# Optimization experiments

Measured on AMD Instinct MI355X. Metric: run time of the kernel, lower is better.

The kernel has to match this reference:

```python
import jax, jax.numpy as jnp
import numpy as np

EPS = 1e-6

def rmsnorm(x, w):
    return x * jax.lax.rsqrt(jnp.mean(x * x, axis=-1, keepdims=True) + EPS) * w

def apply_rope(q, k, freqs_cis):
    # q: (B,T,H,D), k: (B,T,Hkv,D), freqs_cis: (T, D//2, 2) = (cos, sin)
    cos = freqs_cis[None, :, None, :, 0]
    sin = freqs_cis[None, :, None, :, 1]
    def rot(t):
        tr = t.reshape(*t.shape[:-1], t.shape[-1] // 2, 2)
        re, im = tr[..., 0], tr[..., 1]
        out = jnp.stack([re * cos - im * sin, re * sin + im * cos], axis=-1)
        return out.reshape(t.shape)
    return rot(q), rot(k)

def swiglu(x, w1, w2, w3):
    # torch Linear: y = x @ W.T ; SwiGLU: (silu(x W1^T) * (x W3^T)) W2^T
    return (jax.nn.silu(x @ w1.T) * (x @ w3.T)) @ w2.T

def setup_inputs() -> dict:
    key = jax.random.key(0)
    ks = jax.random.split(key, 16)
    B, T, C = 4, 2048, 1024
    H, Hkv, D = 16, 4, 64
    E, Hh = 8, 512
    s = 0.02
    # rotary frequencies (theta=10000)
    inv_freq = 1.0 / (10000.0 ** (np.arange(0, D, 2, dtype=np.float32) / D))
    t = np.arange(T, dtype=np.float32)
    ang = np.outer(t, inv_freq)  # (T, D/2)
    freqs_cis = jnp.asarray(np.stack([np.cos(ang), np.sin(ang)], axis=-1))
    return {
        "x": jax.random.normal(ks[0], (B, T, C), jnp.float32),
        "freqs_cis": freqs_cis,
        "norm1_w": jnp.ones((C,), jnp.float32),
        "wq": jax.random.normal(ks[1], (C, C), jnp.float32) * s,
        "wk": jax.random.normal(ks[2], (Hkv * D, C), jnp.float32) * s,
        "wv": jax.random.normal(ks[3], (Hkv * D, C), jnp.float32) * s,
        "wo": jax.random.normal(ks[4], (C, C), jnp.float32) * s,
        "norm2_w": jnp.ones((C,), jnp.float32),
        "gate_w": jax.random.normal(ks[5], (E, C), jnp.float32) * s,
        "sw1": jax.random.normal(ks[6], (Hh, C), jnp.float32) * s,
        "sw2": jax.random.normal(ks[7], (C, Hh), jnp.float32) * s,
        "sw3": jax.random.normal(ks[8], (Hh, C), jnp.float32) * s,
        "ew1": jax.random.normal(ks[9], (E, Hh, C), jnp.float32) * s,
        "ew2": jax.random.normal(ks[10], (E, C, Hh), jnp.float32) * s,
        "ew3": jax.random.normal(ks[11], (E, Hh, C), jnp.float32) * s,
    }

def reference(x, freqs_cis, norm1_w, wq, wk, wv, wo, norm2_w, gate_w,
              sw1, sw2, sw3, ew1, ew2, ew3):
    B, T, C = x.shape
    H, Hkv = 16, 4
    D = C // H
    n_rep = H // Hkv
    E, top_k = gate_w.shape[0], 2

    # --- attention (GQA + RoPE, causal) ---
    xn = rmsnorm(x, norm1_w)
    q = (xn @ wq.T).reshape(B, T, H, D)
    k = (xn @ wk.T).reshape(B, T, Hkv, D)
    v = (xn @ wv.T).reshape(B, T, Hkv, D)
    q, k = apply_rope(q, k, freqs_cis)
    k = jnp.repeat(k, n_rep, axis=2)
    v = jnp.repeat(v, n_rep, axis=2)
    q, k, v = (t.transpose(0, 2, 1, 3) for t in (q, k, v))  # (B,H,T,D)
    scores = jnp.einsum("bhqd,bhkd->bhqk", q, k) / jnp.sqrt(jnp.float32(D))
    causal = jnp.tril(jnp.ones((T, T), bool))
    scores = jnp.where(causal, scores, jnp.finfo(scores.dtype).min)
    attn = jax.nn.softmax(scores, axis=-1)
    y = jnp.einsum("bhqk,bhkd->bhqd", attn, v)
    y = y.transpose(0, 2, 1, 3).reshape(B, T, C) @ wo.T
    x = x + y

    # --- MoE FFN ---
    xn2 = rmsnorm(x, norm2_w)
    shared = swiglu(xn2, sw1, sw2, sw3)
    router_logits = xn2 @ gate_w.T  # (B,T,E)
    top_logits, top_idx = jax.lax.top_k(router_logits, top_k)
    top_w = jax.nn.softmax(top_logits, axis=-1)  # (B,T,top_k)
    # dense per-expert weight, zero where not selected (same math as masked loop)
    w_full = jnp.sum(jax.nn.one_hot(top_idx, E, dtype=xn2.dtype) * top_w[..., None], axis=-2)  # (B,T,E)
    h = jax.nn.silu(jnp.einsum("btc,ehc->bteh", xn2, ew1)) * jnp.einsum("btc,ehc->bteh", xn2, ew3)
    expert_out = jnp.einsum("bteh,ech,bte->btc", h, ew2, w_full)
    x = x + shared + expert_out
    return x, router_logits
```

## Files before the change

### kernel.cpp

```cpp
#include <hip/hip_runtime.h>
#include <math.h>

typedef __bf16 bf16;
typedef bf16 bf16x8 __attribute__((ext_vector_type(8)));
typedef bf16 bf16x4 __attribute__((ext_vector_type(4)));
typedef float f32x4 __attribute__((ext_vector_type(4)));

#define B_    4
#define T_    2048
#define C_    1024
#define H_    16
#define HKV_  4
#define D_    64
#define HH_   512
#define E_    8
#define MTOK  (B_*T_)
#define MAXTILES 144
#define ROWCAP  (MAXTILES*128)

__device__ __forceinline__ f32x4 mfma16(bf16x8 a, bf16x8 b, f32x4 c) {
  return __builtin_amdgcn_mfma_f32_16x16x32_bf16(a, b, c, 0, 0, 0);
}

#define GLOAD16(gsrc, ldst) \
  __builtin_amdgcn_global_load_lds((const __attribute__((address_space(1))) void*)(gsrc), \
                                   (__attribute__((address_space(3))) void*)(ldst), 16, 0, 0)

#define XCD_SWZ(bx, by) \
  const int _nw  = gridDim.x * gridDim.y; \
  const int _bid = blockIdx.y * gridDim.x + blockIdx.x; \
  const int _swz = (_bid & 7) * (_nw >> 3) + (_bid >> 3); \
  const int bx = _swz % gridDim.x; \
  const int by = _swz / gridDim.x;

struct CastSegs {
  const float* src[10];
  bf16* dst[10];
  int prefix[11];
};
__global__ void cast_all_kernel(CastSegs cs) {
  int i = blockIdx.x * 256 + threadIdx.x;
  if (i >= cs.prefix[10]) return;
  int seg = 0;
  #pragma unroll
  for (int k = 0; k < 9; ++k) if (i >= cs.prefix[k+1]) seg = k+1;
  int j = i - cs.prefix[seg];
  float4 v = reinterpret_cast<const float4*>(cs.src[seg])[j];
  bf16x4 o = { (bf16)v.x, (bf16)v.y, (bf16)v.z, (bf16)v.w };
  reinterpret_cast<bf16x4*>(cs.dst[seg])[j] = o;
}

__global__ void rmsnorm_cast_kernel(const float* __restrict__ x, const float* __restrict__ w,
                                    bf16* __restrict__ out) {
  int row = blockIdx.x;
  const float4* xr = reinterpret_cast<const float4*>(x + (size_t)row * C_);
  float4 v = xr[threadIdx.x];
  float ss = v.x*v.x + v.y*v.y + v.z*v.z + v.w*v.w;
  #pragma unroll
  for (int off = 32; off > 0; off >>= 1) ss += __shfl_down(ss, off);
  __shared__ float red[4];
  if ((threadIdx.x & 63) == 0) red[threadIdx.x >> 6] = ss;
  __syncthreads();
  float tot = red[0] + red[1] + red[2] + red[3];
  float scale = rsqrtf(tot * (1.0f / C_) + 1e-6f);
  float4 wv = reinterpret_cast<const float4*>(w)[threadIdx.x];
  bf16x4 o = { (bf16)(v.x*scale*wv.x), (bf16)(v.y*scale*wv.y),
               (bf16)(v.z*scale*wv.z), (bf16)(v.w*scale*wv.w) };
  reinterpret_cast<bf16x4*>(out + (size_t)row * C_)[threadIdx.x] = o;
}

template<int EPI>
__global__ __launch_bounds__(256, 4)
void gemm_bt(const bf16* __restrict__ A, const bf16* __restrict__ W,
             float* __restrict__ D, const float* __restrict__ SRC,
             const float* __restrict__ RS, int rs_stride,
             int M, int N, int K)
{
  XCD_SWZ(bx, by);
  __shared__ __align__(16) bf16 As[128*32];
  __shared__ __align__(16) bf16 Bs[128*32];
  const int tid  = threadIdx.x;
  const int lane = tid & 63;
  const int wid  = tid >> 6;
  const int wr = wid >> 1, wc = wid & 1;
  const int m0 = by * 128;
  const int n0 = bx * 128;
  const int r  = lane & 15;
  const int kg = lane >> 4;
  const int srow = wid * 32 + (lane >> 2);
  const int scol = (lane & 3) * 8;
  const bf16* gA = A + (size_t)(m0 + srow) * K + scol;
  const bf16* gB = W + (size_t)(n0 + srow) * K + scol;
  bf16* lA = As + wid * 1024;
  bf16* lB = Bs + wid * 1024;

  f32x4 acc[4][4];
  #pragma unroll
  for (int i = 0; i < 4; ++i)
    #pragma unroll
    for (int j = 0; j < 4; ++j) acc[i][j] = f32x4{0.f,0.f,0.f,0.f};

  for (int kk = 0; kk < K; kk += 32) {
    GLOAD16(gA + kk,          lA);
    GLOAD16(gA + 16*K + kk,   lA + 512);
    GLOAD16(gB + kk,          lB);
    GLOAD16(gB + 16*K + kk,   lB + 512);
    __syncthreads();
    bf16x8 a[4], b[4];
    #pragma unroll
    for (int i = 0; i < 4; ++i)
      a[i] = *reinterpret_cast<const bf16x8*>(&As[(wr*64 + i*16 + r)*32 + kg*8]);
    #pragma unroll
    for (int j = 0; j < 4; ++j)
      b[j] = *reinterpret_cast<const bf16x8*>(&Bs[(wc*64 + j*16 + r)*32 + kg*8]);
    #pragma unroll
    for (int i = 0; i < 4; ++i)
      #pragma unroll
      for (int j = 0; j < 4; ++j)
        acc[i][j] = mfma16(a[i], b[j], acc[i][j]);
    __syncthreads();
  }
  const int dr = kg * 4;
  #pragma unroll
  for (int i = 0; i < 4; ++i)
    #pragma unroll
    for (int j = 0; j < 4; ++j)
      #pragma unroll
      for (int rr = 0; rr < 4; ++rr) {
        int m = m0 + wr*64 + i*16 + dr + rr;
        int n = n0 + wc*64 + j*16 + r;
        size_t idx = (size_t)m * N + n;
        float v = acc[i][j][rr];
        if (EPI == 0)      D[idx] = v;
        else if (EPI == 1) D[idx] = SRC[idx] + v;
        else if (EPI == 2) D[idx] += v;
        else               D[idx] += RS[(size_t)m * rs_stride] * v;
      }
}

__global__ __launch_bounds__(256, 4)
void gemm_qkv(const bf16* __restrict__ A, const bf16* __restrict__ W,
              const float* __restrict__ fr,
              bf16* __restrict__ qb, bf16* __restrict__ kb, bf16* __restrict__ vb)
{
  const int K = C_;
  XCD_SWZ(bx, by);
  __shared__ __align__(16) bf16 As[128*32];
  __shared__ __align__(16) bf16 Bs[128*32];
  const int tid  = threadIdx.x;
  const int lane = tid & 63;
  const int wid  = tid >> 6;
  const int wr = wid >> 1, wc = wid & 1;
  const int m0 = by * 128;
  const int n0 = bx * 128;
  const int r  = lane & 15;
  const int kg = lane >> 4;
  const int srow = wid * 32 + (lane >> 2);
  const int scol = (lane & 3) * 8;
  const bf16* gA = A + (size_t)(m0 + srow) * K + scol;
  const bf16* gB = W + (size_t)(n0 + srow) * K + scol;
  bf16* lA = As + wid * 1024;
  bf16* lB = Bs + wid * 1024;

  f32x4 acc[4][4];
  #pragma unroll
  for (int i = 0; i < 4; ++i)
    #pragma unroll
    for (int j = 0; j < 4; ++j) acc[i][j] = f32x4{0.f,0.f,0.f,0.f};

  for (int kk = 0; kk < K; kk += 32) {
    GLOAD16(gA + kk,          lA);
    GLOAD16(gA + 16*K + kk,   lA + 512);
    GLOAD16(gB + kk,          lB);
    GLOAD16(gB + 16*K + kk,   lB + 512);
    __syncthreads();
    bf16x8 a[4], b[4];
    #pragma unroll
    for (int i = 0; i < 4; ++i)
      a[i] = *reinterpret_cast<const bf16x8*>(&As[(wr*64 + i*16 + r)*32 + kg*8]);
    #pragma unroll
    for (int j = 0; j < 4; ++j)
      b[j] = *reinterpret_cast<const bf16x8*>(&Bs[(wc*64 + j*16 + r)*32 + kg*8]);
    #pragma unroll
    for (int i = 0; i < 4; ++i)
      #pragma unroll
      for (int j = 0; j < 4; ++j)
        acc[i][j] = mfma16(a[i], b[j], acc[i][j]);
    __syncthreads();
  }
  const float QSCALE = 0.125f * 1.44269504088896340736f;
  const int dr = kg * 4;
  #pragma unroll
  for (int i = 0; i < 4; ++i)
    #pragma unroll
    for (int j = 0; j < 4; ++j)
      #pragma unroll
      for (int rr = 0; rr < 4; ++rr) {
        int mrow = m0 + wr*64 + i*16 + dr + rr;
        int b  = mrow >> 11, t = mrow & (T_ - 1);
        int n  = n0 + wc*64 + j*16 + r;
        float v = acc[i][j][rr];
        float p = __shfl_xor(v, 1);
        if (n < 1024) {
          float c = fr[t*64 + (n & 62)], s = fr[t*64 + (n & 62) + 1];
          float ov = (n & 1) ? (p*s + v*c) : (v*c - p*s);
          qb[((size_t)(b*H_ + (n >> 6)) * T_ + t) * 64 + (n & 63)] = (bf16)(ov * QSCALE);
        } else if (n < 1280) {
          float c = fr[t*64 + (n & 62)], s = fr[t*64 + (n & 62) + 1];
          float ov = (n & 1) ? (p*s + v*c) : (v*c - p*s);
          kb[((size_t)(b*HKV_ + ((n - 1024) >> 6)) * T_ + t) * 64 + (n & 63)] = (bf16)ov;
        } else {
          vb[((size_t)(b*HKV_ + ((n - 1280) >> 6)) * T_ + t) * 64 + (n & 63)] = (bf16)v;
        }
      }
}

__global__ __launch_bounds__(256, 4)
void gemm_up_all(const bf16* __restrict__ A,
                 const bf16* __restrict__ SW1, const bf16* __restrict__ SW3,
                 const bf16* __restrict__ EW1, const bf16* __restrict__ EW3,
                 size_t wstride, bf16* __restrict__ sb, bf16* __restrict__ sbm,
                 const int* __restrict__ tb, const int* __restrict__ tki)
{
  const int K = C_;
  XCD_SWZ(bx, by);
  const int y = by;
  const bool dense = (y < 64);
  const bf16 *W1, *W3;
  int rowbase;
  bf16* outp;
  if (dense) {
    W1 = SW1; W3 = SW3; rowbase = y * 128; outp = sb;
  } else {
    int ye = y - 64;
    if (ye >= tb[16]) return;
    int g = 0;
    while (ye >= tb[g + 1]) ++g;
    W1 = EW1 + (size_t)(g & 7) * wstride;
    W3 = EW3 + (size_t)(g & 7) * wstride;
    rowbase = ye * 128; outp = sbm;
  }

  __shared__ __align__(16) bf16 As[128*32];
  __shared__ __align__(16) bf16 W1s[64*32];
  __shared__ __align__(16) bf16 W3s[64*32];
  const int tid  = threadIdx.x;
  const int lane = tid & 63;
  const int wid  = tid >> 6;
  const int wr = wid >> 1, wc = wid & 1;
  const int n0 = bx * 64;
  const int r  = lane & 15;
  const int kg = lane >> 4;

  const int sArow = wid * 32 + (lane >> 2);
  int arow0 = dense ? (rowbase + sArow)      : tki[rowbase + sArow];
  int arow1 = dense ? (rowbase + sArow + 16) : tki[rowbase + sArow + 16];
  const int sWrow = n0 + wid * 16 + (lane >> 2);
  const int scol  = (lane & 3) * 8;
  const bf16* gA0 = A  + (size_t)arow0 * K + scol;
  const bf16* gA1 = A  + (size_t)arow1 * K + scol;
  const bf16* gW1 = W1 + (size_t)sWrow * K + scol;
  const bf16* gW3 = W3 + (size_t)sWrow * K + scol;
  bf16* lA  = As  + wid * 1024;
  bf16* lW1 = W1s + wid * 512;
  bf16* lW3 = W3s + wid * 512;

  f32x4 acc1[4][2], acc3[4][2];
  #pragma unroll
  for (int i = 0; i < 4; ++i)
    #pragma unroll
    for (int j = 0; j < 2; ++j) { acc1[i][j] = f32x4{0.f,0.f,0.f,0.f}; acc3[i][j] = f32x4{0.f,0.f,0.f,0.f}; }

  for (int kk = 0; kk < K; kk += 32) {
    GLOAD16(gA0 + kk,       lA);
    GLOAD16(gA1 + kk,       lA + 512);
    GLOAD16(gW1 + kk,       lW1);
    GLOAD16(gW3 + kk,       lW3);
    __syncthreads();
    bf16x8 a[4], w1f[2], w3f[2];
    #pragma unroll
    for (int i = 0; i < 4; ++i)
      a[i] = *reinterpret_cast<const bf16x8*>(&As[(wr*64 + i*16 + r)*32 + kg*8]);
    #pragma unroll
    for (int j = 0; j < 2; ++j) {
      w1f[j] = *reinterpret_cast<const bf16x8*>(&W1s[(wc*32 + j*16 + r)*32 + kg*8]);
      w3f[j] = *reinterpret_cast<const bf16x8*>(&W3s[(wc*32 + j*16 + r)*32 + kg*8]);
    }
    #pragma unroll
    for (int i = 0; i < 4; ++i)
      #pragma unroll
      for (int j = 0; j < 2; ++j) {
        acc1[i][j] = mfma16(a[i], w1f[j], acc1[i][j]);
        acc3[i][j] = mfma16(a[i], w3f[j], acc3[i][j]);
      }
    __syncthreads();
  }
  const int dr = kg * 4;
  #pragma unroll
  for (int i = 0; i < 4; ++i)
    #pragma unroll
    for (int j = 0; j < 2; ++j)
      #pragma unroll
      for (int rr = 0; rr < 4; ++rr) {
        int row = rowbase + wr*64 + i*16 + dr + rr;
        int n = n0 + wc*32 + j*16 + r;
        float v1 = acc1[i][j][rr];
        float v3 = acc3[i][j][rr];
        outp[(size_t)row * HH_ + n] = (bf16)(v1 / (1.f + __expf(-v1)) * v3);
      }
}

__global__ __launch_bounds__(256, 4)
void gemm_down_all(const bf16* __restrict__ Asb, const bf16* __restrict__ Asbm,
                   const bf16* __restrict__ SW2, const bf16* __restrict__ EW2,
                   size_t wstride, float* __restrict__ out, bf16* __restrict__ dwn,
                   const int* __restrict__ tb)
{
  const int K = HH_;
  XCD_SWZ(bx, by);
  const int y = by;
  const bool dense = (y < 64);
  const bf16 *A, *W;
  int rowbase;
  if (dense) {
    A = Asb; W = SW2; rowbase = y * 128;
  } else {
    int ye = y - 64;
    if (ye >= tb[16]) return;
    int g = 0;
    while (ye >= tb[g + 1]) ++g;
    A = Asbm; W = EW2 + (size_t)(g & 7) * wstride;
    rowbase = ye * 128;
  }

  __shared__ __align__(16) bf16 As[128*32];
  __shared__ __align__(16) bf16 Bs[128*32];
  const int tid  = threadIdx.x;
  const int lane = tid & 63;
  const int wid  = tid >> 6;
  const int wr = wid >> 1, wc = wid & 1;
  const int n0 = bx * 128;
  const int r  = lane & 15;
  const int kg = lane >> 4;

  const int srow = wid * 32 + (lane >> 2);
  const int scol = (lane & 3) * 8;
  const bf16* gA = A + (size_t)(rowbase + srow) * K + scol;
  const bf16* gB = W + (size_t)(n0 + srow) * K + scol;
  bf16* lA = As + wid * 1024;
  bf16* lB = Bs + wid * 1024;

  f32x4 acc[4][4];
  #pragma unroll
  for (int i = 0; i < 4; ++i)
    #pragma unroll
    for (int j = 0; j < 4; ++j) acc[i][j] = f32x4{0.f,0.f,0.f,0.f};

  for (int kk = 0; kk < K; kk += 32) {
    GLOAD16(gA + kk,          lA);
    GLOAD16(gA + 16*K + kk,   lA + 512);
    GLOAD16(gB + kk,          lB);
    GLOAD16(gB + 16*K + kk,   lB + 512);
    __syncthreads();
    bf16x8 a[4], b[4];
    #pragma unroll
    for (int i = 0; i < 4; ++i)
      a[i] = *reinterpret_cast<const bf16x8*>(&As[(wr*64 + i*16 + r)*32 + kg*8]);
    #pragma unroll
    for (int j = 0; j < 4; ++j)
      b[j] = *reinterpret_cast<const bf16x8*>(&Bs[(wc*64 + j*16 + r)*32 + kg*8]);
    #pragma unroll
    for (int i = 0; i < 4; ++i)
      #pragma unroll
      for (int j = 0; j < 4; ++j)
        acc[i][j] = mfma16(a[i], b[j], acc[i][j]);
    __syncthreads();
  }
  const int dr = kg * 4;
  #pragma unroll
  for (int i = 0; i < 4; ++i)
    #pragma unroll
    for (int j = 0; j < 4; ++j)
      #pragma unroll
      for (int rr = 0; rr < 4; ++rr) {
        int row = rowbase + wr*64 + i*16 + dr + rr;
        int n = n0 + wc*64 + j*16 + r;
        float v = acc[i][j][rr];
        if (dense) out[(size_t)row * C_ + n] += v;
        else       dwn[(size_t)row * C_ + n] = (bf16)v;
      }
}

__global__ void moe_scatter_kernel(const bf16* __restrict__ dwn,
                                   const int* __restrict__ t2s,
                                   const float* __restrict__ t2w,
                                   float* __restrict__ out)
{
  int t = blockIdx.x;
  int c = threadIdx.x;
  int s0 = t2s[2*t], s1 = t2s[2*t+1];
  float w0 = t2w[2*t], w1 = t2w[2*t+1];
  bf16x4 a = reinterpret_cast<const bf16x4*>(dwn + (size_t)s0 * C_)[c];
  bf16x4 b = reinterpret_cast<const bf16x4*>(dwn + (size_t)s1 * C_)[c];
  float4* o = reinterpret_cast<float4*>(out + (size_t)t * C_);
  float4 v = o[c];
  v.x += w0 * (float)a[0] + w1 * (float)b[0];
  v.y += w0 * (float)a[1] + w1 * (float)b[1];
  v.z += w0 * (float)a[2] + w1 * (float)b[2];
  v.w += w0 * (float)a[3] + w1 * (float)b[3];
  o[c] = v;
}

__global__ void transpose_vb_kernel(const bf16* __restrict__ vb, bf16* __restrict__ vt) {
  int idx = blockIdx.x * 256 + threadIdx.x;
  const int total = B_ * HKV_ * 64 * T_;
  if (idx >= total) return;
  int t   = idx & (T_ - 1);
  int d   = (idx >> 11) & 63;
  int kvh = (idx >> 17) & 3;
  int b   = idx >> 19;
  vt[idx] = vb[((size_t)(b*HKV_ + kvh) * T_ + t) * 64 + d];
}

__global__ __launch_bounds__(256, 2)
void flash_attn_kernel(const bf16* __restrict__ Q, const bf16* __restrict__ K,
                       const bf16* __restrict__ VT, bf16* __restrict__ Y)
{
  __shared__ __align__(16) bf16 Klds[64*64];
  __shared__ __align__(16) bf16 Vlds[64*64];
  __shared__ bf16 Plds[4][2][16][72];
  const int tid  = threadIdx.x;
  const int lane = tid & 63;
  const int wid  = tid >> 6;
  const int bid  = blockIdx.x;
  const int gw   = (bid & 7) * 64 + (bid >> 3);
  const int i    = gw & 31;
  const int kvh  = (gw >> 5) & 3;
  const int b    = gw >> 7;
  const int h    = kvh * 4 + wid;
  const int r = lane & 15;
  const int g = lane >> 4;

  const bf16* kptr = K  + ((size_t)(b*HKV_ + kvh) * T_) * 64;
  const bf16* vptr = VT + ((size_t)(b*HKV_ + kvh) * 64) * T_;

  const int srow  = tid >> 3;
  const int schnk = (tid & 7) ^ (srow & 7);
  bf16* kd0 = Klds + wid * 512;
  bf16* kd1 = Klds + 2048 + wid * 512;
  bf16* vd0 = Vlds + wid * 512;
  bf16* vd1 = Vlds + 2048 + wid * 512;

  const int swz0 = ((g    ) ^ (r & 7)) * 8;
  const int swz4 = ((g + 4) ^ (r & 7)) * 8;

  bf16x8 ones;
  #pragma unroll
  for (int z = 0; z < 8; ++z) ones[z] = (bf16)1.0f;

  #pragma unroll
  for (int pi = 0; pi < 2; ++pi) {
    const int qt = pi == 0 ? (63 - i) : i;
    const int qbase = qt * 32;
    const bf16* qptr = Q + ((size_t)(b*H_ + h) * T_ + qbase) * 64;

    bf16x8 aq[2][2];
    #pragma unroll
    for (int u = 0; u < 2; ++u) {
      aq[u][0] = *reinterpret_cast<const bf16x8*>(qptr + (size_t)(u*16 + r) * 64 + g*8);
      aq[u][1] = *reinterpret_cast<const bf16x8*>(qptr + (size_t)(u*16 + r) * 64 + 32 + g*8);
    }

    f32x4 o[2][4], ol[2];
    #pragma unroll
    for (int u = 0; u < 2; ++u) {
      ol[u] = f32x4{0.f,0.f,0.f,0.f};
      #pragma unroll
      for (int q = 0; q < 4; ++q) o[u][q] = f32x4{0.f,0.f,0.f,0.f};
    }

    for (int k0 = 0; k0 < qbase + 32; k0 += 64) {
      GLOAD16(kptr + (size_t)(k0 + srow)      * 64 + schnk*8, kd0);
      GLOAD16(kptr + (size_t)(k0 + 32 + srow) * 64 + schnk*8, kd1);
      GLOAD16(vptr + (size_t)srow        * T_ + k0 + schnk*8, vd0);
      GLOAD16(vptr + (size_t)(32 + srow) * T_ + k0 + schnk*8, vd1);
      __syncthreads();
      f32x4 s[2][4];
      __builtin_amdgcn_s_setprio(1);
      #pragma unroll
      for (int c = 0; c < 4; ++c) {
        const bf16* kb = &Klds[(c*16 + r) * 64];
        bf16x8 kf0 = *reinterpret_cast<const bf16x8*>(kb + swz0);
        bf16x8 kf1 = *reinterpret_cast<const bf16x8*>(kb + swz4);
        #pragma unroll
        for (int u = 0; u < 2; ++u) {
          s[u][c] = f32x4{0.f,0.f,0.f,0.f};
          s[u][c] = mfma16(aq[u][0], kf0, s[u][c]);
          s[u][c] = mfma16(aq[u][1], kf1, s[u][c]);
        }
      }
      __builtin_amdgcn_s_setprio(0);
      #pragma unroll
      for (int u = 0; u < 2; ++u) {
        if (k0 + 63 > qbase + u*16) {
          #pragma unroll
          for (int c = 0; c < 4; ++c)
            #pragma unroll
            for (int rr = 0; rr < 4; ++rr) {
              int q = qbase + u*16 + g*4 + rr;
              int j = k0 + c*16 + r;
              if (j > q) s[u][c][rr] = -__builtin_inff();
            }
        }
      }
      #pragma unroll
      for (int u = 0; u < 2; ++u)
        #pragma unroll
        for (int c = 0; c < 4; ++c)
          #pragma unroll
          for (int rr = 0; rr < 4; ++rr)
            Plds[wid][u][g*4+rr][c*16+r] = (bf16)__builtin_amdgcn_exp2f(s[u][c][rr]);
      bf16x8 pa[2][2];
      #pragma unroll
      for (int u = 0; u < 2; ++u) {
        pa[u][0] = *reinterpret_cast<const bf16x8*>(&Plds[wid][u][r][g*8]);
        pa[u][1] = *reinterpret_cast<const bf16x8*>(&Plds[wid][u][r][32 + g*8]);
      }
      __builtin_amdgcn_s_setprio(1);
      #pragma unroll
      for (int dt = 0; dt < 4; ++dt) {
        const bf16* vb = &Vlds[(dt*16 + r) * 64];
        bf16x8 vf0 = *reinterpret_cast<const bf16x8*>(vb + swz0);
        bf16x8 vf1 = *reinterpret_cast<const bf16x8*>(vb + swz4);
        #pragma unroll
        for (int u = 0; u < 2; ++u) {
          o[u][dt] = mfma16(pa[u][0], vf0, o[u][dt]);
          o[u][dt] = mfma16(pa[u][1], vf1, o[u][dt]);
        }
      }
      #pragma unroll
      for (int u = 0; u < 2; ++u) {
        ol[u] = mfma16(pa[u][0], ones, ol[u]);
        ol[u] = mfma16(pa[u][1], ones, ol[u]);
      }
      __builtin_amdgcn_s_setprio(0);
      __syncthreads();
    }
    #pragma unroll
    for (int u = 0; u < 2; ++u)
      #pragma unroll
      for (int rr = 0; rr < 4; ++rr) {
        float inv = 1.0f / ol[u][rr];
        int t = qbase + u*16 + g*4 + rr;
        bf16* yrow = Y + ((size_t)(b*T_ + t)) * C_ + h*64;
        #pragma unroll
        for (int dt = 0; dt < 4; ++dt)
          yrow[dt*16 + r] = (bf16)(o[u][dt][rr] * inv);
      }
  }
}

__global__ void rms2_router_kernel(const float* __restrict__ x2, const float* __restrict__ nw,
                                   const float* __restrict__ gwf,
                                   bf16* __restrict__ xn_out,
                                   float* __restrict__ logits_out,
                                   int* __restrict__ t2i, float* __restrict__ t2w)
{
  int t = blockIdx.x * 4 + (threadIdx.x >> 6);
  int lane = threadIdx.x & 63;
  const float4* xr = reinterpret_cast<const float4*>(x2 + (size_t)t * C_) + lane * 4;
  float4 v[4];
  float ss = 0.f;
  #pragma unroll
  for (int i = 0; i < 4; ++i) {
    v[i] = xr[i];
    ss += v[i].x*v[i].x + v[i].y*v[i].y + v[i].z*v[i].z + v[i].w*v[i].w;
  }
  #pragma unroll
  for (int off = 32; off > 0; off >>= 1) ss += __shfl_xor(ss, off);
  float scale = rsqrtf(ss * (1.0f / C_) + 1e-6f);
  const float4* nr = reinterpret_cast<const float4*>(nw) + lane * 4;
  float xn[16];
  #pragma unroll
  for (int i = 0; i < 4; ++i) {
    float4 wv = nr[i];
    xn[4*i+0] = v[i].x * scale * wv.x;
    xn[4*i+1] = v[i].y * scale * wv.y;
    xn[4*i+2] = v[i].z * scale * wv.z;
    xn[4*i+3] = v[i].w * scale * wv.w;
  }
  {
    bf16x8 o0, o1;
    #pragma unroll
    for (int i = 0; i < 8; ++i) { o0[i] = (bf16)xn[i]; o1[i] = (bf16)xn[8+i]; }
    bf16x8* dst = reinterpret_cast<bf16x8*>(xn_out + (size_t)t * C_ + lane * 16);
    dst[0] = o0;
    dst[1] = o1;
  }
  float lg[8];
  #pragma unroll
  for (int e = 0; e < 8; ++e) {
    const float4* gr = reinterpret_cast<const float4*>(gwf + (size_t)e * C_) + lane * 4;
    float d = 0.f;
    #pragma unroll
    for (int i = 0; i < 4; ++i) {
      float4 gv = gr[i];
      d += xn[4*i+0]*gv.x + xn[4*i+1]*gv.y + xn[4*i+2]*gv.z + xn[4*i+3]*gv.w;
    }
    #pragma unroll
    for (int off = 1; off < 64; off <<= 1) d += __shfl_xor(d, off);
    lg[e] = d;
  }
  if (lane == 0) {
    #pragma unroll
    for (int e = 0; e < 8; ++e) logits_out[(size_t)t*8 + e] = lg[e];
    int i0 = 0; float b0 = lg[0];
    #pragma unroll
    for (int e = 1; e < 8; ++e) if (lg[e] > b0) { b0 = lg[e]; i0 = e; }
    int i1 = -1; float b1 = -__builtin_inff();
    #pragma unroll
    for (int e = 0; e < 8; ++e) if (e != i0 && lg[e] > b1) { b1 = lg[e]; i1 = e; }
    float w0s = 1.f / (1.f + __expf(b1 - b0));
    float w1s = 1.f - w0s;
    t2i[2*t] = i0;  t2i[2*t+1] = i1;
    t2w[2*t] = w0s; t2w[2*t+1] = w1s;
  }
}

__global__ void moe_build_kernel(const int* __restrict__ t2i, const float* __restrict__ t2w,
                                 int* __restrict__ cnt, int* __restrict__ tb,
                                 int* __restrict__ tki, float* __restrict__ tkw,
                                 int* __restrict__ t2s)
{
  __shared__ int lcnt[16], lbase[17], lcur[16];
  const int tid = threadIdx.x;
  if (tid < 16) { lcnt[tid] = 0; lcur[tid] = 0; }
  __syncthreads();
  for (int t = tid; t < MTOK; t += 1024) {
    atomicAdd(&lcnt[t2i[2*t]],     1);
    atomicAdd(&lcnt[8 + t2i[2*t+1]], 1);
  }
  __syncthreads();
  if (tid == 0) {
    int acc = 0;
    for (int g = 0; g < 16; ++g) { lbase[g] = acc; acc += (lcnt[g] + 127) >> 7; }
    lbase[16] = acc;
    for (int g = 0; g <= 16; ++g) tb[g] = lbase[g];
  }
  if (tid < 16) cnt[tid] = lcnt[tid];
  __syncthreads();
  for (int t = tid; t < MTOK; t += 1024) {
    #pragma unroll
    for (int j = 0; j < 2; ++j) {
      int g = 8*j + t2i[2*t + j];
      int p = atomicAdd(&lcur[g], 1);
      int slot = lbase[g] * 128 + p;
      tki[slot] = t;
      tkw[slot] = t2w[2*t + j];
      t2s[2*t + j] = slot;
    }
  }
  __syncthreads();
  {
    int g = tid >> 6, lane = tid & 63;
    int cs = lcnt[g];
    int ce = (cs + 127) & ~127;
    for (int p = cs + lane; p < ce; p += 64) {
      int slot = lbase[g] * 128 + p;
      tki[slot] = 0;
      tkw[slot] = 0.f;
    }
  }
}

__global__ void silu_mul_kernel(const float* __restrict__ a, const float* __restrict__ bsrc,
                                bf16* __restrict__ out, int n4)
{
  int i = blockIdx.x * 256 + threadIdx.x;
  if (i >= n4) return;
  float4 av = reinterpret_cast<const float4*>(a)[i];
  float4 bv = reinterpret_cast<const float4*>(bsrc)[i];
  bf16x4 o = { (bf16)(av.x / (1.f + __expf(-av.x)) * bv.x),
               (bf16)(av.y / (1.f + __expf(-av.y)) * bv.y),
               (bf16)(av.z / (1.f + __expf(-av.z)) * bv.z),
               (bf16)(av.w / (1.f + __expf(-av.w)) * bv.w) };
  reinterpret_cast<bf16x4*>(out)[i] = o;
}

__global__ void build_wfull_kernel(const int* __restrict__ t2i, const float* __restrict__ t2w,
                                   float* __restrict__ wfull) {
  int t = blockIdx.x * 256 + threadIdx.x;
  if (t >= MTOK) return;
  #pragma unroll
  for (int e = 0; e < 8; ++e) wfull[(size_t)t*8 + e] = 0.f;
  wfull[(size_t)t*8 + t2i[2*t]]   = t2w[2*t];
  wfull[(size_t)t*8 + t2i[2*t+1]] = t2w[2*t+1];
}

extern "C" void kernel_launch(void* const* d_in, const int* in_sizes, int n_in,
                              void* d_out, int out_size, void* d_ws, size_t ws_size,
                              hipStream_t stream)
{
  const float* x    = (const float*)d_in[0];
  const float* fr   = (const float*)d_in[1];
  const float* n1w  = (const float*)d_in[2];
  const float* wq   = (const float*)d_in[3];
  const float* wk   = (const float*)d_in[4];
  const float* wv   = (const float*)d_in[5];
  const float* wo   = (const float*)d_in[6];
  const float* n2w  = (const float*)d_in[7];
  const float* gw   = (const float*)d_in[8];
  const float* sw1  = (const float*)d_in[9];
  const float* sw2  = (const float*)d_in[10];
  const float* sw3  = (const float*)d_in[11];
  const float* ew1  = (const float*)d_in[12];
  const float* ew2  = (const float*)d_in[13];
  const float* ew3  = (const float*)d_in[14];

  float* out    = (float*)d_out;
  float* logits = out + (size_t)MTOK * C_;

  char* ws = (char*)d_ws;
  size_t off = 0;
  auto alloc = [&](size_t bytes) { size_t o = off; off += (bytes + 255) & ~(size_t)255; return o; };

  bf16* wq_b  = (bf16*)(ws + alloc((size_t)C_*C_*2));
  bf16* wk_b  = (bf16*)(ws + alloc((size_t)HKV_*D_*C_*2));
  bf16* wv_b  = (bf16*)(ws + alloc((size_t)HKV_*D_*C_*2));
  bf16* wo_b  = (bf16*)(ws + alloc((size_t)C_*C_*2));
  bf16* sw1_b = (bf16*)(ws + alloc((size_t)HH_*C_*2));
  bf16* sw3_b = (bf16*)(ws + alloc((size_t)HH_*C_*2));
  bf16* sw2_b = (bf16*)(ws + alloc((size_t)C_*HH_*2));
  bf16* ew1_b = (bf16*)(ws + alloc((size_t)E_*HH_*C_*2));
  bf16* ew2_b = (bf16*)(ws + alloc((size_t)E_*C_*HH_*2));
  bf16* ew3_b = (bf16*)(ws + alloc((size_t)E_*HH_*C_*2));
  bf16* xn_b  = (bf16*)(ws + alloc((size_t)MTOK*C_*2));
  float* wfull= (float*)(ws + alloc((size_t)MTOK*E_*4));
  int*   t2i  = (int*)  (ws + alloc((size_t)MTOK*2*4));
  float* t2w  = (float*)(ws + alloc((size_t)MTOK*2*4));
  int*   t2s  = (int*)  (ws + alloc((size_t)MTOK*2*4));
  int*   tki  = (int*)  (ws + alloc((size_t)ROWCAP*4));
  float* tkw  = (float*)(ws + alloc((size_t)ROWCAP*4));
  int*   cnt  = (int*)  (ws + alloc(32*4));
  int*   tb   = (int*)  (ws + alloc(32*4));

  const size_t POOLSZ = 75497472;
  size_t poolbase = alloc(POOLSZ);
  char* pool = ws + poolbase;
  bf16* qb = (bf16*)(pool);
  bf16* kb = (bf16*)(pool + 33554432);
  bf16* vb = (bf16*)(pool + 41943040);
  bf16* vT = (bf16*)(pool + 50331648);
  bf16* yb = (bf16*)(pool + 58720256);
  bf16* sb  = (bf16*)(pool);
  bf16* sbm = (bf16*)(pool + 8388608);
  bf16* dwn = (bf16*)(pool + 8388608 + 18874368);
  float* g1 = (float*)pool;
  float* g3 = g1 + (size_t)MTOK*HH_;
  bf16*  sbf = (bf16*)(pool + 58720256);

  bool sparse_ok = (ws_size >= off);

  {
    CastSegs cs;
    const float* srcs[10] = { wq, wk, wv, wo, sw1, sw3, sw2, ew1, ew2, ew3 };
    bf16* dsts[10] = { wq_b, wk_b, wv_b, wo_b, sw1_b, sw3_b, sw2_b, ew1_b, ew2_b, ew3_b };
    int n4s[10] = { C_*C_/4, HKV_*D_*C_/4, HKV_*D_*C_/4, C_*C_/4,
                    HH_*C_/4, HH_*C_/4, C_*HH_/4,
                    E_*HH_*C_/4, E_*C_*HH_/4, E_*HH_*C_/4 };
    int acc = 0;
    for (int k = 0; k < 10; ++k) { cs.src[k] = srcs[k]; cs.dst[k] = dsts[k]; cs.prefix[k] = acc; acc += n4s[k]; }
    cs.prefix[10] = acc;
    cast_all_kernel<<<(acc + 255)/256, 256, 0, stream>>>(cs);
  }

  rmsnorm_cast_kernel<<<MTOK, 256, 0, stream>>>(x, n1w, xn_b);

  gemm_qkv<<<dim3(1536/128, MTOK/128), 256, 0, stream>>>(xn_b, wq_b, fr, qb, kb, vb);
  transpose_vb_kernel<<<(B_*HKV_*64*T_)/256, 256, 0, stream>>>(vb, vT);

  flash_attn_kernel<<<B_*HKV_*(T_/64), 256, 0, stream>>>(qb, kb, vT, yb);

  gemm_bt<1><<<dim3(C_/128, MTOK/128), 256, 0, stream>>>(yb, wo_b, out, x, nullptr, 0, MTOK, C_, C_);

  rms2_router_kernel<<<MTOK/4, 256, 0, stream>>>(out, n2w, gw, xn_b, logits, t2i, t2w);

  if (sparse_ok) {
    moe_build_kernel<<<1, 1024, 0, stream>>>(t2i, t2w, cnt, tb, tki, tkw, t2s);
    gemm_up_all<<<dim3(HH_/64, 64 + MAXTILES), 256, 0, stream>>>(xn_b,
        sw1_b, sw3_b, ew1_b, ew3_b, (size_t)HH_*C_, sb, sbm, tb, tki);
    gemm_down_all<<<dim3(C_/128, 64 + MAXTILES), 256, 0, stream>>>(sb, sbm,
        sw2_b, ew2_b, (size_t)C_*HH_, out, dwn, tb);
    moe_scatter_kernel<<<MTOK, 256, 0, stream>>>(dwn, t2s, t2w, out);
  } else {
    gemm_up_all<<<dim3(HH_/64, 64), 256, 0, stream>>>(xn_b,
        sw1_b, sw3_b, ew1_b, ew3_b, (size_t)HH_*C_, sb, sbm, tb, tki);
    gemm_bt<2><<<dim3(C_/128, MTOK/128), 256, 0, stream>>>(sb, sw2_b, out, nullptr, nullptr, 0, MTOK, C_, HH_);
    build_wfull_kernel<<<MTOK/256, 256, 0, stream>>>(t2i, t2w, wfull);
    for (int e = 0; e < E_; ++e) {
      const bf16* e1 = ew1_b + (size_t)e * HH_ * C_;
      const bf16* e3 = ew3_b + (size_t)e * HH_ * C_;
      const bf16* e2 = ew2_b + (size_t)e * C_ * HH_;
      gemm_bt<0><<<dim3(HH_/128, MTOK/128), 256, 0, stream>>>(xn_b, e1, g1, nullptr, nullptr, 0, MTOK, HH_, C_);
      gemm_bt<0><<<dim3(HH_/128, MTOK/128), 256, 0, stream>>>(xn_b, e3, g3, nullptr, nullptr, 0, MTOK, HH_, C_);
      silu_mul_kernel<<<((MTOK*HH_/4) + 255)/256, 256, 0, stream>>>(g1, g3, sbf, MTOK*HH_/4);
      gemm_bt<3><<<dim3(C_/128, MTOK/128), 256, 0, stream>>>(sbf, e2, out, nullptr, wfull + e, E_, MTOK, C_, HH_);
    }
  }
}
```

Measured before the change: 371.2 us.

## Double K-tile depth to 64 with XOR-swizzled LDS layout in all GEMMs

All four GEMM kernels now stage a K-slice of 64 per iteration instead of 32, which halves the number of barrier pairs and global-to-LDS rounds per output tile. The LDS rows widen to 64 elements and use an XOR swizzle of the 16-byte chunk index by row, applied on both the store and the fragment reads, to avoid bank conflicts. The cost is doubled shared memory per block, which may lower occupancy under the 4-blocks-per-CU launch bound.

```diff
diff --git a/kernel.cpp b/kernel.cpp
--- a/kernel.cpp
+++ b/kernel.cpp
@@ -77,8 +77,8 @@
              int M, int N, int K)
 {
   XCD_SWZ(bx, by);
-  __shared__ __align__(16) bf16 As[128*32];
-  __shared__ __align__(16) bf16 Bs[128*32];
+  __shared__ __align__(16) bf16 As[128*64];
+  __shared__ __align__(16) bf16 Bs[128*64];
   const int tid  = threadIdx.x;
   const int lane = tid & 63;
   const int wid  = tid >> 6;
@@ -87,12 +87,12 @@
   const int n0 = bx * 128;
   const int r  = lane & 15;
   const int kg = lane >> 4;
-  const int srow = wid * 32 + (lane >> 2);
-  const int scol = (lane & 3) * 8;
-  const bf16* gA = A + (size_t)(m0 + srow) * K + scol;
-  const bf16* gB = W + (size_t)(n0 + srow) * K + scol;
-  bf16* lA = As + wid * 1024;
-  bf16* lB = Bs + wid * 1024;
+  const int sr8 = lane >> 3;
+  const int sc  = ((lane & 7) ^ sr8) * 8;
+  const bf16* gA = A + (size_t)(m0 + wid*32 + sr8) * K + sc;
+  const bf16* gB = W + (size_t)(n0 + wid*32 + sr8) * K + sc;
+  bf16* lA = As + wid * 2048;
+  bf16* lB = Bs + wid * 2048;
 
   f32x4 acc[4][4];
   #pragma unroll
@@ -100,24 +100,29 @@
     #pragma unroll
     for (int j = 0; j < 4; ++j) acc[i][j] = f32x4{0.f,0.f,0.f,0.f};
 
-  for (int kk = 0; kk < K; kk += 32) {
-    GLOAD16(gA + kk,          lA);
-    GLOAD16(gA + 16*K + kk,   lA + 512);
-    GLOAD16(gB + kk,          lB);
-    GLOAD16(gB + 16*K + kk,   lB + 512);
+  for (int kk = 0; kk < K; kk += 64) {
+    #pragma unroll
+    for (int p = 0; p < 4; ++p) {
+      GLOAD16(gA + (size_t)(8*p) * K + kk, lA + p*512);
+      GLOAD16(gB + (size_t)(8*p) * K + kk, lB + p*512);
+    }
     __syncthreads();
-    bf16x8 a[4], b[4];
-    #pragma unroll
-    for (int i = 0; i < 4; ++i)
-      a[i] = *reinterpret_cast<const bf16x8*>(&As[(wr*64 + i*16 + r)*32 + kg*8]);
-    #pragma unroll
-    for (int j = 0; j < 4; ++j)
-      b[j] = *reinterpret_cast<const bf16x8*>(&Bs[(wc*64 + j*16 + r)*32 + kg*8]);
-    #pragma unroll
-    for (int i = 0; i < 4; ++i)
+    #pragma unroll
+    for (int ks = 0; ks < 2; ++ks) {
+      const int sz = (((ks << 2) | kg) ^ (r & 7)) * 8;
+      bf16x8 a[4], b[4];
+      #pragma unroll
+      for (int i = 0; i < 4; ++i)
+        a[i] = *reinterpret_cast<const bf16x8*>(&As[(wr*64 + i*16 + r)*64 + sz]);
       #pragma unroll
       for (int j = 0; j < 4; ++j)
-        acc[i][j] = mfma16(a[i], b[j], acc[i][j]);
+        b[j] = *reinterpret_cast<const bf16x8*>(&Bs[(wc*64 + j*16 + r)*64 + sz]);
+      #pragma unroll
+      for (int i = 0; i < 4; ++i)
+        #pragma unroll
+        for (int j = 0; j < 4; ++j)
+          acc[i][j] = mfma16(a[i], b[j], acc[i][j]);
+    }
     __syncthreads();
   }
   const int dr = kg * 4;
@@ -145,8 +150,8 @@
 {
   const int K = C_;
   XCD_SWZ(bx, by);
-  __shared__ __align__(16) bf16 As[128*32];
-  __shared__ __align__(16) bf16 Bs[128*32];
+  __shared__ __align__(16) bf16 As[128*64];
+  __shared__ __align__(16) bf16 Bs[128*64];
   const int tid  = threadIdx.x;
   const int lane = tid & 63;
   const int wid  = tid >> 6;
@@ -155,12 +160,12 @@
   const int n0 = bx * 128;
   const int r  = lane & 15;
   const int kg = lane >> 4;
-  const int srow = wid * 32 + (lane >> 2);
-  const int scol = (lane & 3) * 8;
-  const bf16* gA = A + (size_t)(m0 + srow) * K + scol;
-  const bf16* gB = W + (size_t)(n0 + srow) * K + scol;
-  bf16* lA = As + wid * 1024;
-  bf16* lB = Bs + wid * 1024;
+  const int sr8 = lane >> 3;
+  const int sc  = ((lane & 7) ^ sr8) * 8;
+  const bf16* gA = A + (size_t)(m0 + wid*32 + sr8) * K + sc;
+  const bf16* gB = W + (size_t)(n0 + wid*32 + sr8) * K + sc;
+  bf16* lA = As + wid * 2048;
+  bf16* lB = Bs + wid * 2048;
 
   f32x4 acc[4][4];
   #pragma unroll
@@ -168,24 +173,29 @@
     #pragma unroll
     for (int j = 0; j < 4; ++j) acc[i][j] = f32x4{0.f,0.f,0.f,0.f};
 
-  for (int kk = 0; kk < K; kk += 32) {
-    GLOAD16(gA + kk,          lA);
-    GLOAD16(gA + 16*K + kk,   lA + 512);
-    GLOAD16(gB + kk,          lB);
-    GLOAD16(gB + 16*K + kk,   lB + 512);
+  for (int kk = 0; kk < K; kk += 64) {
+    #pragma unroll
+    for (int p = 0; p < 4; ++p) {
+      GLOAD16(gA + (size_t)(8*p) * K + kk, lA + p*512);
+      GLOAD16(gB + (size_t)(8*p) * K + kk, lB + p*512);
+    }
     __syncthreads();
-    bf16x8 a[4], b[4];
-    #pragma unroll
-    for (int i = 0; i < 4; ++i)
-      a[i] = *reinterpret_cast<const bf16x8*>(&As[(wr*64 + i*16 + r)*32 + kg*8]);
-    #pragma unroll
-    for (int j = 0; j < 4; ++j)
-      b[j] = *reinterpret_cast<const bf16x8*>(&Bs[(wc*64 + j*16 + r)*32 + kg*8]);
-    #pragma unroll
-    for (int i = 0; i < 4; ++i)
+    #pragma unroll
+    for (int ks = 0; ks < 2; ++ks) {
+      const int sz = (((ks << 2) | kg) ^ (r & 7)) * 8;
+      bf16x8 a[4], b[4];
+      #pragma unroll
+      for (int i = 0; i < 4; ++i)
+        a[i] = *reinterpret_cast<const bf16x8*>(&As[(wr*64 + i*16 + r)*64 + sz]);
       #pragma unroll
       for (int j = 0; j < 4; ++j)
-        acc[i][j] = mfma16(a[i], b[j], acc[i][j]);
+        b[j] = *reinterpret_cast<const bf16x8*>(&Bs[(wc*64 + j*16 + r)*64 + sz]);
+      #pragma unroll
+      for (int i = 0; i < 4; ++i)
+        #pragma unroll
+        for (int j = 0; j < 4; ++j)
+          acc[i][j] = mfma16(a[i], b[j], acc[i][j]);
+    }
     __syncthreads();
   }
   const float QSCALE = 0.125f * 1.44269504088896340736f;
@@ -241,9 +251,9 @@
     rowbase = ye * 128; outp = sbm;
   }
 
-  __shared__ __align__(16) bf16 As[128*32];
-  __shared__ __align__(16) bf16 W1s[64*32];
-  __shared__ __align__(16) bf16 W3s[64*32];
+  __shared__ __align__(16) bf16 As[128*64];
+  __shared__ __align__(16) bf16 W1s[64*64];
+  __shared__ __align__(16) bf16 W3s[64*64];
   const int tid  = threadIdx.x;
   const int lane = tid & 63;
   const int wid  = tid >> 6;
@@ -251,19 +261,20 @@
   const int n0 = bx * 64;
   const int r  = lane & 15;
   const int kg = lane >> 4;
-
-  const int sArow = wid * 32 + (lane >> 2);
-  int arow0 = dense ? (rowbase + sArow)      : tki[rowbase + sArow];
-  int arow1 = dense ? (rowbase + sArow + 16) : tki[rowbase + sArow + 16];
-  const int sWrow = n0 + wid * 16 + (lane >> 2);
-  const int scol  = (lane & 3) * 8;
-  const bf16* gA0 = A  + (size_t)arow0 * K + scol;
-  const bf16* gA1 = A  + (size_t)arow1 * K + scol;
-  const bf16* gW1 = W1 + (size_t)sWrow * K + scol;
-  const bf16* gW3 = W3 + (size_t)sWrow * K + scol;
-  bf16* lA  = As  + wid * 1024;
-  bf16* lW1 = W1s + wid * 512;
-  bf16* lW3 = W3s + wid * 512;
+  const int sr8 = lane >> 3;
+  const int sc  = ((lane & 7) ^ sr8) * 8;
+
+  int ar[4];
+  #pragma unroll
+  for (int p = 0; p < 4; ++p) {
+    int rw = rowbase + wid*32 + p*8 + sr8;
+    ar[p] = dense ? rw : tki[rw];
+  }
+  const bf16* gW1 = W1 + (size_t)(n0 + wid*16 + sr8) * K + sc;
+  const bf16* gW3 = W3 + (size_t)(n0 + wid*16 + sr8) * K + sc;
+  bf16* lA  = As  + wid * 2048;
+  bf16* lW1 = W1s + wid * 1024;
+  bf16* lW3 = W3s + wid * 1024;
 
   f32x4 acc1[4][2], acc3[4][2];
   #pragma unroll
@@ -271,28 +282,36 @@
     #pragma unroll
     for (int j = 0; j < 2; ++j) { acc1[i][j] = f32x4{0.f,0.f,0.f,0.f}; acc3[i][j] = f32x4{0.f,0.f,0.f,0.f}; }
 
-  for (int kk = 0; kk < K; kk += 32) {
-    GLOAD16(gA0 + kk,       lA);
-    GLOAD16(gA1 + kk,       lA + 512);
-    GLOAD16(gW1 + kk,       lW1);
-    GLOAD16(gW3 + kk,       lW3);
+  for (int kk = 0; kk < K; kk += 64) {
+    #pragma unroll
+    for (int p = 0; p < 4; ++p)
+      GLOAD16(A + (size_t)ar[p] * K + sc + kk, lA + p*512);
+    #pragma unroll
+    for (int p = 0; p < 2; ++p) {
+      GLOAD16(gW1 + (size_t)(8*p) * K + kk, lW1 + p*512);
+      GLOAD16(gW3 + (size_t)(8*p) * K + kk, lW3 + p*512);
+    }
     __syncthreads();
-    bf16x8 a[4], w1f[2], w3f[2];
-    #pragma unroll
-    for (int i = 0; i < 4; ++i)
-      a[i] = *reinterpret_cast<const bf16x8*>(&As[(wr*64 + i*16 + r)*32 + kg*8]);
-    #pragma unroll
-    for (int j = 0; j < 2; ++j) {
-      w1f[j] = *reinterpret_cast<const bf16x8*>(&W1s[(wc*32 + j*16 + r)*32 + kg*8]);
-      w3f[j] = *reinterpret_cast<const bf16x8*>(&W3s[(wc*32 + j*16 + r)*32 + kg*8]);
-    }
-    #pragma unroll
-    for (int i = 0; i < 4; ++i)
+    #pragma unroll
+    for (int ks = 0; ks < 2; ++ks) {
+      const int sz = (((ks << 2) | kg) ^ (r & 7)) * 8;
+      bf16x8 a[4], w1f[2], w3f[2];
+      #pragma unroll
+      for (int i = 0; i < 4; ++i)
+        a[i] = *reinterpret_cast<const bf16x8*>(&As[(wr*64 + i*16 + r)*64 + sz]);
       #pragma unroll
       for (int j = 0; j < 2; ++j) {
-        acc1[i][j] = mfma16(a[i], w1f[j], acc1[i][j]);
-        acc3[i][j] = mfma16(a[i], w3f[j], acc3[i][j]);
-      }
+        w1f[j] = *reinterpret_cast<const bf16x8*>(&W1s[(wc*32 + j*16 + r)*64 + sz]);
+        w3f[j] = *reinterpret_cast<const bf16x8*>(&W3s[(wc*32 + j*16 + r)*64 + sz]);
+      }
+      #pragma unroll
+      for (int i = 0; i < 4; ++i)
+        #pragma unroll
+        for (int j = 0; j < 2; ++j) {
+          acc1[i][j] = mfma16(a[i], w1f[j], acc1[i][j]);
+          acc3[i][j] = mfma16(a[i], w3f[j], acc3[i][j]);
+        }
+    }
     __syncthreads();
   }
   const int dr = kg * 4;
@@ -333,8 +352,8 @@
     rowbase = ye * 128;
   }
 
-  __shared__ __align__(16) bf16 As[128*32];
-  __shared__ __align__(16) bf16 Bs[128*32];
+  __shared__ __align__(16) bf16 As[128*64];
+  __shared__ __align__(16) bf16 Bs[128*64];
   const int tid  = threadIdx.x;
   const int lane = tid & 63;
   const int wid  = tid >> 6;
@@ -342,13 +361,12 @@
   const int n0 = bx * 128;
   const int r  = lane & 15;
   const int kg = lane >> 4;
-
-  const int srow = wid * 32 + (lane >> 2);
-  const int scol = (lane & 3) * 8;
-  const bf16* gA = A + (size_t)(rowbase + srow) * K + scol;
-  const bf16* gB = W + (size_t)(n0 + srow) * K + scol;
-  bf16* lA = As + wid * 1024;
-  bf16* lB = Bs + wid * 1024;
+  const int sr8 = lane >> 3;
+  const int sc  = ((lane & 7) ^ sr8) * 8;
+  const bf16* gA = A + (size_t)(rowbase + wid*32 + sr8) * K + sc;
+  const bf16* gB = W + (size_t)(n0 + wid*32 + sr8) * K + sc;
+  bf16* lA = As + wid * 2048;
+  bf16* lB = Bs + wid * 2048;
 
   f32x4 acc[4][4];
   #pragma unroll
@@ -356,24 +374,29 @@
     #pragma unroll
     for (int j = 0; j < 4; ++j) acc[i][j] = f32x4{0.f,0.f,0.f,0.f};
 
-  for (int kk = 0; kk < K; kk += 32) {
-    GLOAD16(gA + kk,          lA);
-    GLOAD16(gA + 16*K + kk,   lA + 512);
-    GLOAD16(gB + kk,          lB);
-    GLOAD16(gB + 16*K + kk,   lB + 512);
+  for (int kk = 0; kk < K; kk += 64) {
+    #pragma unroll
+    for (int p = 0; p < 4; ++p) {
+      GLOAD16(gA + (size_t)(8*p) * K + kk, lA + p*512);
+      GLOAD16(gB + (size_t)(8*p) * K + kk, lB + p*512);
+    }
     __syncthreads();
-    bf16x8 a[4], b[4];
-    #pragma unroll
-    for (int i = 0; i < 4; ++i)
-      a[i] = *reinterpret_cast<const bf16x8*>(&As[(wr*64 + i*16 + r)*32 + kg*8]);
-    #pragma unroll
-    for (int j = 0; j < 4; ++j)
-      b[j] = *reinterpret_cast<const bf16x8*>(&Bs[(wc*64 + j*16 + r)*32 + kg*8]);
-    #pragma unroll
-    for (int i = 0; i < 4; ++i)
+    #pragma unroll
+    for (int ks = 0; ks < 2; ++ks) {
+      const int sz = (((ks << 2) | kg) ^ (r & 7)) * 8;
+      bf16x8 a[4], b[4];
+      #pragma unroll
+      for (int i = 0; i < 4; ++i)
+        a[i] = *reinterpret_cast<const bf16x8*>(&As[(wr*64 + i*16 + r)*64 + sz]);
       #pragma unroll
       for (int j = 0; j < 4; ++j)
-        acc[i][j] = mfma16(a[i], b[j], acc[i][j]);
+        b[j] = *reinterpret_cast<const bf16x8*>(&Bs[(wc*64 + j*16 + r)*64 + sz]);
+      #pragma unroll
+      for (int i = 0; i < 4; ++i)
+        #pragma unroll
+        for (int j = 0; j < 4; ++j)
+          acc[i][j] = mfma16(a[i], b[j], acc[i][j]);
+    }
     __syncthreads();
   }
   const int dr = kg * 4;
```

Result: faster. 342.1 us (-7.8%).
